# Kernel tuning notes

Measured on AMD Instinct MI355X. Metric: run time of the kernel, lower is better.

Reference implementation:

```python
import jax, jax.numpy as jnp
import numpy as np

FRACTION = 0.33  # from attn_type='query_selector_0.33'


def setup_inputs() -> dict:
    key = jax.random.key(0)
    k1, k2, k3, k4 = jax.random.split(key, 4)
    B, L, DIM_VAL, DIM_ATTN = 8, 4096, 64, 64
    scale = 1.0 / np.sqrt(DIM_VAL).astype(np.float32)
    x = jax.random.normal(k1, (B, L, DIM_VAL), dtype=jnp.float32)
    Wq = jax.random.normal(k2, (DIM_VAL, DIM_ATTN), dtype=jnp.float32) * scale
    Wk = jax.random.normal(k3, (DIM_VAL, DIM_ATTN), dtype=jnp.float32) * scale
    Wv = jax.random.normal(k4, (DIM_VAL, DIM_VAL), dtype=jnp.float32) * scale
    return {"x": x, "Wq": Wq, "Wk": Wk, "Wv": Wv}


def reference(x, Wq, Wk, Wv):
    # Projections (bias-free Linears)
    Q = jnp.einsum('bld,de->ble', x, Wq)  # [B, L, Da]
    K = jnp.einsum('bld,de->ble', x, Wk)  # [B, L, Da]
    V = jnp.einsum('bld,de->ble', x, Wv)  # [B, L, Dv]

    B, L_Q, Da = Q.shape
    l_Q = int((1.0 - FRACTION) * L_Q)  # static: shapes known at trace time

    # keys.topk(l_Q, dim=1).values -> per-channel top-l_Q along seq; mean over them
    K_top = jax.lax.top_k(jnp.swapaxes(K, 1, 2), l_Q)[0]  # [B, Da, l_Q]
    K_reduce = K_top.mean(axis=-1)                         # [B, Da]

    # score each query against the reduced key; pick top-l_Q queries
    sqk = jnp.einsum('bd,bld->bl', K_reduce, Q)            # [B, L_Q]
    indices = jax.lax.top_k(sqk, l_Q)[1]                   # [B, l_Q] int32

    # gather sampled queries
    Q_sample = jnp.take_along_axis(Q, indices[:, :, None], axis=1)  # [B, l_Q, Da]

    # dense attention for the sampled queries only
    scores = jnp.einsum('bqd,bkd->bqk', Q_sample, K) / jnp.sqrt(jnp.asarray(Da, Q.dtype))
    attn = jax.nn.softmax(scores, axis=-1)                 # [B, l_Q, L]
    out_sel = jnp.einsum('bqk,bkv->bqv', attn, V)          # [B, l_Q, Dv]

    # mean-filled result, scatter attention outputs to selected rows
    mean_values = V.mean(axis=-2)                          # [B, Dv]
    result = jnp.broadcast_to(mean_values[:, None, :], (B, L_Q, V.shape[-1]))
    result = result.at[jnp.arange(B)[:, None], indices].set(out_sel)
    return result
```

## Files before the change

kernel.cpp:

```cpp
#include <hip/hip_runtime.h>
#include <hip/hip_bf16.h>
#include <math.h>

#define BATCH 8
#define SEQ   4096
#define DIM   64
#define LQ    2744
#define QPB   128
#define NQB   22
#define QPAD  2816
#define KS    4
#define L2E   1.4426950408889634f
#define QSC   0.1803368801111204f

typedef _Float16 half8 __attribute__((ext_vector_type(8)));
typedef short    bs8   __attribute__((ext_vector_type(8)));
typedef float    fx16  __attribute__((ext_vector_type(16)));
typedef unsigned short ushort_t;

union UH { uint4 u4; half8 h; };
union UB { unsigned u[4]; uint4 u4; bs8 s; };

__device__ __forceinline__ unsigned pack_bf16(float a, float b) {
    __hip_bfloat162 h = __float22bfloat162_rn(make_float2(a, b));
    union { __hip_bfloat162 h; unsigned u; } cv; cv.h = h; return cv.u;
}

__device__ __forceinline__ unsigned f2sort(float f) {
    unsigned u = __float_as_uint(f);
    return (u & 0x80000000u) ? ~u : (u | 0x80000000u);
}
__device__ __forceinline__ float sort2f(unsigned u) {
    return __uint_as_float((u & 0x80000000u) ? (u & 0x7FFFFFFFu) : ~u);
}

__device__ void radix_select_4096(const unsigned* u, int k, unsigned* hist,
                                  unsigned* scan, unsigned* res) {
    const int t = threadIdx.x;
    if (t == 0) { res[0] = 0u; res[1] = (unsigned)k; }
    for (int pass = 3; pass >= 0; --pass) {
        const int shift = pass * 8;
        hist[t] = 0u;
        __syncthreads();
        const unsigned pref  = res[0];
        const unsigned kk    = res[1];
        const unsigned hmask = (pass == 3) ? 0u : (0xFFFFFFFFu << (shift + 8));
        for (int i = t; i < 4096; i += 256) {
            unsigned ui = u[i];
            if ((ui & hmask) == pref) atomicAdd(&hist[(ui >> shift) & 255u], 1u);
        }
        __syncthreads();
        const unsigned h = hist[t];
        unsigned s = h;
        scan[t] = s;
        __syncthreads();
#pragma unroll
        for (int ofs = 1; ofs < 256; ofs <<= 1) {
            unsigned add = (t + ofs < 256) ? scan[t + ofs] : 0u;
            __syncthreads();
            s += add;
            scan[t] = s;
            __syncthreads();
        }
        if (s >= kk && (s - h) < kk) {
            res[0] = pref | ((unsigned)t << shift);
            res[1] = kk - (s - h);
        }
        __syncthreads();
    }
}

__global__ __launch_bounds__(256) void proj_kernel(
    const float* __restrict__ x,  const float* __restrict__ Wq,
    const float* __restrict__ Wk, const float* __restrict__ Wv,
    float* __restrict__ Q, float* __restrict__ Kt,
    _Float16* __restrict__ Qh, _Float16* __restrict__ Kh,
    ushort_t* __restrict__ Vt, float* __restrict__ pmean) {
    const int rt = blockIdx.x, b = blockIdx.y, t = threadIdx.x;
    __shared__ float4 xs4[64 * 17];
    __shared__ float  red[4][64];
    {
        const float4* xg = (const float4*)(x + ((size_t)b * SEQ + rt * 64) * DIM);
        for (int i = 0; i < 4; ++i) {
            int s = t + 256 * i;
            xs4[(s >> 4) * 17 + (s & 15)] = xg[s];
        }
    }
    __syncthreads();
    const int ch = t & 63, rg = t >> 6;
    float accq[16], acck[16], accv[16];
#pragma unroll
    for (int i = 0; i < 16; ++i) { accq[i] = 0.f; acck[i] = 0.f; accv[i] = 0.f; }
    for (int dc = 0; dc < 4; ++dc) {
        float wq[16], wk[16], wv[16];
#pragma unroll
        for (int dd = 0; dd < 16; ++dd) {
            int d = dc * 16 + dd;
            wq[dd] = Wq[d * 64 + ch]; wk[dd] = Wk[d * 64 + ch]; wv[dd] = Wv[d * 64 + ch];
        }
        for (int r = 0; r < 16; ++r) {
            const int row = rg * 16 + r;
            const float4* xr = &xs4[row * 17 + dc * 4];
            float xv[16];
            float4 a0 = xr[0], a1 = xr[1], a2 = xr[2], a3 = xr[3];
            xv[0]=a0.x; xv[1]=a0.y; xv[2]=a0.z; xv[3]=a0.w;
            xv[4]=a1.x; xv[5]=a1.y; xv[6]=a1.z; xv[7]=a1.w;
            xv[8]=a2.x; xv[9]=a2.y; xv[10]=a2.z; xv[11]=a2.w;
            xv[12]=a3.x; xv[13]=a3.y; xv[14]=a3.z; xv[15]=a3.w;
#pragma unroll
            for (int dd = 0; dd < 16; ++dd) {
                accq[r] = fmaf(xv[dd], wq[dd], accq[r]);
                acck[r] = fmaf(xv[dd], wk[dd], acck[r]);
                accv[r] = fmaf(xv[dd], wv[dd], accv[r]);
            }
        }
    }
    const int rowbase = rt * 64 + rg * 16;
    float sv = 0.f;
#pragma unroll
    for (int r = 0; r < 16; ++r) {
        size_t o = ((size_t)b * SEQ + rowbase + r) * DIM + ch;
        Q[o]  = accq[r];
        Qh[o] = (_Float16)(accq[r] * QSC);
        Kh[o] = (_Float16)acck[r];
        sv += accv[r];
    }
    float4* ktp = (float4*)(Kt + ((size_t)b * 64 + ch) * SEQ + rowbase);
    ktp[0] = make_float4(acck[0], acck[1], acck[2], acck[3]);
    ktp[1] = make_float4(acck[4], acck[5], acck[6], acck[7]);
    ktp[2] = make_float4(acck[8], acck[9], acck[10], acck[11]);
    ktp[3] = make_float4(acck[12], acck[13], acck[14], acck[15]);
    {
        unsigned pk[8];
#pragma unroll
        for (int i = 0; i < 8; ++i) pk[i] = pack_bf16(accv[2*i], accv[2*i+1]);
        uint4* vp = (uint4*)(Vt + ((size_t)(b * 64 + ch)) * SEQ + rowbase);
        vp[0] = make_uint4(pk[0], pk[1], pk[4], pk[5]);
        vp[1] = make_uint4(pk[2], pk[3], pk[6], pk[7]);
    }
    red[rg][ch] = sv;
    __syncthreads();
    if (rg == 0)
        pmean[((size_t)b * 64 + ch) * 64 + rt] =
            red[0][ch] + red[1][ch] + red[2][ch] + red[3][ch];
}

__global__ __launch_bounds__(256) void kmean_kernel(const float* __restrict__ Kt,
                                                    const float* __restrict__ pmean,
                                                    float* __restrict__ Kred,
                                                    float* __restrict__ meanfin) {
    __shared__ unsigned u[4096];
    __shared__ unsigned hist[256];
    __shared__ unsigned scan[256];
    __shared__ unsigned res[2];
    __shared__ float rsum[4];
    const int bc = blockIdx.x, t = threadIdx.x;
    if (t < 64) {
        float v = pmean[(size_t)bc * 64 + t];
        for (int m = 1; m < 64; m <<= 1) v += __shfl_xor(v, m, 64);
        if (t == 0) meanfin[bc] = v * (1.0f / (float)SEQ);
    }
    const float4* c4 = (const float4*)(Kt + (size_t)bc * SEQ);
    for (int i = t; i < 1024; i += 256) {
        float4 v = c4[i];
        u[i*4+0] = f2sort(v.x); u[i*4+1] = f2sort(v.y);
        u[i*4+2] = f2sort(v.z); u[i*4+3] = f2sort(v.w);
    }
    __syncthreads();
    radix_select_4096(u, LQ, hist, scan, res);
    const unsigned Tu = res[0];
    const int krem = (int)res[1];
    float loc = 0.f;
    for (int i = t; i < 4096; i += 256)
        if (u[i] > Tu) loc += sort2f(u[i]);
    for (int msk = 1; msk < 64; msk <<= 1) loc += __shfl_xor(loc, msk, 64);
    if ((t & 63) == 0) rsum[t >> 6] = loc;
    __syncthreads();
    if (t == 0) {
        float s = rsum[0] + rsum[1] + rsum[2] + rsum[3] + (float)krem * sort2f(Tu);
        Kred[bc] = s / (float)LQ;
    }
}

__global__ __launch_bounds__(256) void sqk_kernel(const float* __restrict__ Q,
                                                  const float* __restrict__ Kred,
                                                  float* __restrict__ sqk) {
    const int b = blockIdx.y, l = blockIdx.x * 256 + threadIdx.x;
    __shared__ float kr[64];
    if (threadIdx.x < 64) kr[threadIdx.x] = Kred[b * 64 + threadIdx.x];
    __syncthreads();
    const float4* q = (const float4*)(Q + ((size_t)b * SEQ + l) * DIM);
    float s = 0.f;
#pragma unroll
    for (int i = 0; i < 16; ++i) {
        float4 v = q[i];
        s = fmaf(v.x, kr[i*4+0], s); s = fmaf(v.y, kr[i*4+1], s);
        s = fmaf(v.z, kr[i*4+2], s); s = fmaf(v.w, kr[i*4+3], s);
    }
    sqk[b * SEQ + l] = s;
}

__global__ __launch_bounds__(256) void select_kernel(const float* __restrict__ sqk,
                                                     int* __restrict__ sel,
                                                     int* __restrict__ inv) {
    __shared__ unsigned u[4096];
    __shared__ unsigned hist[256];
    __shared__ unsigned scan[256];
    __shared__ unsigned res[2];
    __shared__ int eq_idx[256];
    __shared__ int cnts[2];
    const int b = blockIdx.x, t = threadIdx.x;
    const float* col = sqk + (size_t)b * SEQ;
    int* invb = inv + (size_t)b * SEQ;
    for (int i = t; i < 4096; i += 256) {
        u[i] = f2sort(col[i]);
        invb[i] = -1;
    }
    if (t < 2) cnts[t] = 0;
    __syncthreads();
    radix_select_4096(u, LQ, hist, scan, res);
    const unsigned Tu = res[0];
    const int krem = (int)res[1];
    int* selb = sel + b * QPAD;
    for (int i = t; i < 4096; i += 256) {
        unsigned ui = u[i];
        if (ui > Tu) {
            int p = atomicAdd(&cnts[0], 1);
            selb[p] = i;
            invb[i] = p;
        } else if (ui == Tu) {
            int p = atomicAdd(&cnts[1], 1);
            if (p < 256) eq_idx[p] = i;
        }
    }
    __syncthreads();
    if (t == 0) {
        int ng = cnts[0];
        int ne = cnts[1] < 256 ? cnts[1] : 256;
        for (int i = 1; i < ne; ++i) {
            int v = eq_idx[i], j = i - 1;
            while (j >= 0 && eq_idx[j] > v) { eq_idx[j+1] = eq_idx[j]; --j; }
            eq_idx[j+1] = v;
        }
        for (int j = 0; j < krem; ++j) {
            selb[ng + j] = eq_idx[j];
            invb[eq_idx[j]] = ng + j;
        }
    }
    __syncthreads();
    if (t < QPAD - LQ) selb[LQ + t] = selb[LQ - 1];
}

__global__ __launch_bounds__(256, 3) void attn_kernel(
    const ushort_t* __restrict__ Qh, const ushort_t* __restrict__ Kh,
    const ushort_t* __restrict__ Vt, const int* __restrict__ sel,
    float* __restrict__ pl, float* __restrict__ pout) {
    const int qt = blockIdx.x, ks = blockIdx.y, b = blockIdx.z;
    const int t = threadIdx.x, w = t >> 6, lane = t & 63;
    const int col = lane & 31, h = lane >> 5;

    __shared__ ushort_t Ktile[2][32 * 64];
    __shared__ ushort_t Vtile[2][32 * 64];

    half8 qf[4];
    {
        const int q = qt * QPB + w * 32 + col;
        const int row = sel[b * QPAD + q];
        const uint4* qg = (const uint4*)(Qh + ((size_t)b * SEQ + row) * DIM);
#pragma unroll
        for (int m = 0; m < 4; ++m) { UH u; u.u4 = qg[2 * m + h]; qf[m] = u.h; }
    }

    int koff[4], voff[4];
#pragma unroll
    for (int m = 0; m < 4; ++m)
        koff[m] = col * 64 + 8 * ((2 * m + h) ^ (col & 7));
#pragma unroll
    for (int i = 0; i < 4; ++i)
        voff[i] = col * 64 + 8 * ((i * 2 + h) ^ (col & 7));

    fx16 O0, O1;
#pragma unroll
    for (int r = 0; r < 16; ++r) { O0[r] = 0.f; O1[r] = 0.f; }
    float l = 0.f;

    const int srow = t >> 3, sgr = t & 7;
    const int lg = sgr ^ (srow & 7);
    const int vD = lg >> 2, vc = (lg >> 1) & 1, vh = lg & 1;
    const size_t kgbase = ((size_t)b * SEQ + ks * 1024 + srow) * DIM + 8 * lg;
    const size_t vgbase = ((size_t)(b * DIM + srow + 32 * vD)) * SEQ
                          + ks * 1024 + vc * 16 + vh * 8;

    uint4 kreg = *(const uint4*)(Kh + kgbase);
    uint4 vreg = *(const uint4*)(Vt + vgbase);

    for (int tile = 0; tile < 32; ++tile) {
        const int buf = tile & 1;
        *(uint4*)&Ktile[buf][srow * 64 + sgr * 8] = kreg;
        *(uint4*)&Vtile[buf][srow * 64 + sgr * 8] = vreg;
        __syncthreads();
        if (tile < 31) {
            kreg = *(const uint4*)(Kh + kgbase + (size_t)(tile + 1) * 32 * DIM);
            vreg = *(const uint4*)(Vt + vgbase + (size_t)(tile + 1) * 32);
        }
        fx16 S;
#pragma unroll
        for (int r = 0; r < 16; ++r) S[r] = 0.f;
#pragma unroll
        for (int m = 0; m < 4; ++m) {
            UH kf;
            kf.u4 = *(const uint4*)&Ktile[buf][koff[m]];
            S = __builtin_amdgcn_mfma_f32_32x32x16_f16(kf.h, qf[m], S, 0, 0, 0);
        }
        float p[16];
#pragma unroll
        for (int r = 0; r < 16; ++r) p[r] = exp2f(S[r]);
#pragma unroll
        for (int r = 0; r < 16; ++r) l += p[r];
        UB A0, A1;
#pragma unroll
        for (int v = 0; v < 4; ++v) {
            A0.u[v] = pack_bf16(p[2 * v],     p[2 * v + 1]);
            A1.u[v] = pack_bf16(p[8 + 2 * v], p[8 + 2 * v + 1]);
        }
#pragma unroll
        for (int D = 0; D < 2; ++D) {
            fx16& O = D ? O1 : O0;
#pragma unroll
            for (int c = 0; c < 2; ++c) {
                UB vf;
                vf.u4 = *(const uint4*)&Vtile[buf][voff[D * 2 + c]];
                O = __builtin_amdgcn_mfma_f32_32x32x16_bf16(c ? A1.s : A0.s, vf.s, O, 0, 0, 0);
            }
        }
    }

    l += __shfl_xor(l, 32);

    const int qg0 = qt * QPB + w * 32;
    const size_t base = (size_t)b * QPAD + qg0;
#pragma unroll
    for (int D = 0; D < 2; ++D) {
        const fx16& O = D ? O1 : O0;
#pragma unroll
        for (int r = 0; r < 16; ++r) {
            const int q = (r & 3) + 8 * (r >> 2) + 4 * h;
            atomicAdd(&pout[(base + q) * DIM + D * 32 + col], O[r]);
        }
    }
    if (h == 0) atomicAdd(&pl[base + col], l);
}

__global__ __launch_bounds__(256) void comb_kernel(
    const float* __restrict__ pl, const float* __restrict__ pout,
    const int* __restrict__ inv, const float* __restrict__ meanfin,
    float* __restrict__ out) {
    const int idx = blockIdx.x * 256 + threadIdx.x;
    const int b = idx >> 16;
    const int rc = idx & 65535;
    const int row = rc >> 4, c = rc & 15;
    const int p = inv[b * SEQ + row];
    float4 o;
    if (p >= 0) {
        const size_t s0 = (size_t)b * QPAD + p;
        const float invl = 1.0f / pl[s0];
        float4 a = ((const float4*)(pout + s0 * DIM))[c];
        o = make_float4(a.x * invl, a.y * invl, a.z * invl, a.w * invl);
    } else {
        o = make_float4(meanfin[b * 64 + c * 4 + 0], meanfin[b * 64 + c * 4 + 1],
                        meanfin[b * 64 + c * 4 + 2], meanfin[b * 64 + c * 4 + 3]);
    }
    ((float4*)out)[idx] = o;
}

extern "C" void kernel_launch(void* const* d_in, const int* in_sizes, int n_in,
                              void* d_out, int out_size, void* d_ws, size_t ws_size,
                              hipStream_t stream) {
    const float* x  = (const float*)d_in[0];
    const float* Wq = (const float*)d_in[1];
    const float* Wk = (const float*)d_in[2];
    const float* Wv = (const float*)d_in[3];
    float* out = (float*)d_out;
    char* wsb  = (char*)d_ws;

    float*    Q       = (float*)(wsb);
    _Float16* Qh      = (_Float16*)(wsb + 8388608);
    _Float16* Kh      = (_Float16*)(wsb + 12582912);
    ushort_t* Vt      = (ushort_t*)(wsb + 16777216);
    float*    pmean   = (float*)(wsb + 20971520);
    float*    meanfin = (float*)(wsb + 21102592);
    float*    Kred    = (float*)(wsb + 21104640);
    float*    sqk     = (float*)(wsb + 21106688);
    int*      sel     = (int*)(wsb + 21237760);
    int*      inv     = (int*)(wsb + 21327872);
    float*    Kt      = (float*)(wsb + 21458944);
    float*    pout    = (float*)(wsb + 21458944);
    float*    pl      = (float*)(wsb + 21458944 + 5767168);

    proj_kernel  <<<dim3(64, 8),          256, 0, stream>>>(x, Wq, Wk, Wv, Q, Kt,
                                                            Qh, Kh, Vt, pmean);
    kmean_kernel <<<512,                  256, 0, stream>>>(Kt, pmean, Kred, meanfin);
    sqk_kernel   <<<dim3(16, 8),          256, 0, stream>>>(Q, Kred, sqk);
    select_kernel<<<8,                    256, 0, stream>>>(sqk, sel, inv);
    hipMemsetAsync(pout, 0, 5767168 + 90112, stream);
    attn_kernel  <<<dim3(NQB, KS, BATCH), 256, 0, stream>>>((const ushort_t*)Qh,
                                                            (const ushort_t*)Kh,
                                                            Vt, sel, pl, pout);
    comb_kernel  <<<2048,                 256, 0, stream>>>(pl, pout, inv, meanfin, out);
}
```

Baseline: 195.0 us.

## Double attention key splits, fuse query scoring into select, widen selection blocks

Raises the key-split factor from 4 to 8, so the attention grid has twice as many blocks, each covering half as many key tiles. Folds the query-scoring kernel into the selection kernel, removing one launch and the sqk buffer round trip. Runs the radix-select kernels with 1024 threads instead of 256 to speed up their histogram passes. Also swaps in a manual bf16 round-to-nearest pack and the raw exp2 builtin in the attention loop. In exchange, more atomic accumulation into the shared partial outputs, and the 8-block select kernel still has very little parallelism.

```diff
diff --git a/kernel.cpp b/kernel.cpp
--- a/kernel.cpp
+++ b/kernel.cpp
@@ -9,7 +9,7 @@
 #define QPB   128
 #define NQB   22
 #define QPAD  2816
-#define KS    4
+#define KS    8
 #define L2E   1.4426950408889634f
 #define QSC   0.1803368801111204f
 
@@ -22,8 +22,10 @@
 union UB { unsigned u[4]; uint4 u4; bs8 s; };
 
 __device__ __forceinline__ unsigned pack_bf16(float a, float b) {
-    __hip_bfloat162 h = __float22bfloat162_rn(make_float2(a, b));
-    union { __hip_bfloat162 h; unsigned u; } cv; cv.h = h; return cv.u;
+    unsigned ua = __float_as_uint(a), ub = __float_as_uint(b);
+    ua += 0x7FFFu + ((ua >> 16) & 1u);
+    ub += 0x7FFFu + ((ub >> 16) & 1u);
+    return (ua >> 16) | (ub & 0xFFFF0000u);
 }
 
 __device__ __forceinline__ unsigned f2sort(float f) {
@@ -34,35 +36,34 @@
     return __uint_as_float((u & 0x80000000u) ? (u & 0x7FFFFFFFu) : ~u);
 }
 
+template <int NT>
 __device__ void radix_select_4096(const unsigned* u, int k, unsigned* hist,
                                   unsigned* scan, unsigned* res) {
     const int t = threadIdx.x;
     if (t == 0) { res[0] = 0u; res[1] = (unsigned)k; }
     for (int pass = 3; pass >= 0; --pass) {
         const int shift = pass * 8;
-        hist[t] = 0u;
+        if (t < 256) hist[t] = 0u;
         __syncthreads();
         const unsigned pref  = res[0];
         const unsigned kk    = res[1];
         const unsigned hmask = (pass == 3) ? 0u : (0xFFFFFFFFu << (shift + 8));
-        for (int i = t; i < 4096; i += 256) {
+        for (int i = t; i < 4096; i += NT) {
             unsigned ui = u[i];
             if ((ui & hmask) == pref) atomicAdd(&hist[(ui >> shift) & 255u], 1u);
         }
         __syncthreads();
-        const unsigned h = hist[t];
-        unsigned s = h;
-        scan[t] = s;
+        unsigned h = 0u, s = 0u;
+        if (t < 256) { h = hist[t]; s = h; scan[t] = s; }
         __syncthreads();
 #pragma unroll
         for (int ofs = 1; ofs < 256; ofs <<= 1) {
-            unsigned add = (t + ofs < 256) ? scan[t + ofs] : 0u;
+            unsigned add = (t < 256 && t + ofs < 256) ? scan[t + ofs] : 0u;
             __syncthreads();
-            s += add;
-            scan[t] = s;
+            if (t < 256) { s += add; scan[t] = s; }
             __syncthreads();
         }
-        if (s >= kk && (s - h) < kk) {
+        if (t < 256 && s >= kk && (s - h) < kk) {
             res[0] = pref | ((unsigned)t << shift);
             res[1] = kk - (s - h);
         }
@@ -133,7 +134,11 @@
     {
         unsigned pk[8];
 #pragma unroll
-        for (int i = 0; i < 8; ++i) pk[i] = pack_bf16(accv[2*i], accv[2*i+1]);
+        for (int i = 0; i < 8; ++i) {
+            __hip_bfloat162 h2 = __float22bfloat162_rn(make_float2(accv[2*i], accv[2*i+1]));
+            union { __hip_bfloat162 h; unsigned u; } cv; cv.h = h2;
+            pk[i] = cv.u;
+        }
         uint4* vp = (uint4*)(Vt + ((size_t)(b * 64 + ch)) * SEQ + rowbase);
         vp[0] = make_uint4(pk[0], pk[1], pk[4], pk[5]);
         vp[1] = make_uint4(pk[2], pk[3], pk[6], pk[7]);
@@ -145,15 +150,15 @@
             red[0][ch] + red[1][ch] + red[2][ch] + red[3][ch];
 }
 
-__global__ __launch_bounds__(256) void kmean_kernel(const float* __restrict__ Kt,
-                                                    const float* __restrict__ pmean,
-                                                    float* __restrict__ Kred,
-                                                    float* __restrict__ meanfin) {
+__global__ __launch_bounds__(1024) void kmean_kernel(const float* __restrict__ Kt,
+                                                     const float* __restrict__ pmean,
+                                                     float* __restrict__ Kred,
+                                                     float* __restrict__ meanfin) {
     __shared__ unsigned u[4096];
     __shared__ unsigned hist[256];
     __shared__ unsigned scan[256];
     __shared__ unsigned res[2];
-    __shared__ float rsum[4];
+    __shared__ float rsum[16];
     const int bc = blockIdx.x, t = threadIdx.x;
     if (t < 64) {
         float v = pmean[(size_t)bc * 64 + t];
@@ -161,68 +166,62 @@
         if (t == 0) meanfin[bc] = v * (1.0f / (float)SEQ);
     }
     const float4* c4 = (const float4*)(Kt + (size_t)bc * SEQ);
-    for (int i = t; i < 1024; i += 256) {
-        float4 v = c4[i];
-        u[i*4+0] = f2sort(v.x); u[i*4+1] = f2sort(v.y);
-        u[i*4+2] = f2sort(v.z); u[i*4+3] = f2sort(v.w);
-    }
-    __syncthreads();
-    radix_select_4096(u, LQ, hist, scan, res);
+    if (t < 1024) {
+        float4 v = c4[t];
+        u[t*4+0] = f2sort(v.x); u[t*4+1] = f2sort(v.y);
+        u[t*4+2] = f2sort(v.z); u[t*4+3] = f2sort(v.w);
+    }
+    __syncthreads();
+    radix_select_4096<1024>(u, LQ, hist, scan, res);
     const unsigned Tu = res[0];
     const int krem = (int)res[1];
     float loc = 0.f;
-    for (int i = t; i < 4096; i += 256)
+    for (int i = t; i < 4096; i += 1024)
         if (u[i] > Tu) loc += sort2f(u[i]);
     for (int msk = 1; msk < 64; msk <<= 1) loc += __shfl_xor(loc, msk, 64);
     if ((t & 63) == 0) rsum[t >> 6] = loc;
     __syncthreads();
     if (t == 0) {
-        float s = rsum[0] + rsum[1] + rsum[2] + rsum[3] + (float)krem * sort2f(Tu);
+        float s = (float)krem * sort2f(Tu);
+        for (int i = 0; i < 16; ++i) s += rsum[i];
         Kred[bc] = s / (float)LQ;
     }
 }
 
-__global__ __launch_bounds__(256) void sqk_kernel(const float* __restrict__ Q,
-                                                  const float* __restrict__ Kred,
-                                                  float* __restrict__ sqk) {
-    const int b = blockIdx.y, l = blockIdx.x * 256 + threadIdx.x;
-    __shared__ float kr[64];
-    if (threadIdx.x < 64) kr[threadIdx.x] = Kred[b * 64 + threadIdx.x];
-    __syncthreads();
-    const float4* q = (const float4*)(Q + ((size_t)b * SEQ + l) * DIM);
-    float s = 0.f;
-#pragma unroll
-    for (int i = 0; i < 16; ++i) {
-        float4 v = q[i];
-        s = fmaf(v.x, kr[i*4+0], s); s = fmaf(v.y, kr[i*4+1], s);
-        s = fmaf(v.z, kr[i*4+2], s); s = fmaf(v.w, kr[i*4+3], s);
-    }
-    sqk[b * SEQ + l] = s;
-}
-
-__global__ __launch_bounds__(256) void select_kernel(const float* __restrict__ sqk,
-                                                     int* __restrict__ sel,
-                                                     int* __restrict__ inv) {
+__global__ __launch_bounds__(1024) void select_kernel(const float* __restrict__ Q,
+                                                      const float* __restrict__ Kred,
+                                                      int* __restrict__ sel,
+                                                      int* __restrict__ inv) {
     __shared__ unsigned u[4096];
     __shared__ unsigned hist[256];
     __shared__ unsigned scan[256];
     __shared__ unsigned res[2];
+    __shared__ float kr[64];
     __shared__ int eq_idx[256];
     __shared__ int cnts[2];
     const int b = blockIdx.x, t = threadIdx.x;
-    const float* col = sqk + (size_t)b * SEQ;
+    if (t < 64) kr[t] = Kred[b * 64 + t];
+    if (t < 2) cnts[t] = 0;
     int* invb = inv + (size_t)b * SEQ;
-    for (int i = t; i < 4096; i += 256) {
-        u[i] = f2sort(col[i]);
-        invb[i] = -1;
-    }
-    if (t < 2) cnts[t] = 0;
-    __syncthreads();
-    radix_select_4096(u, LQ, hist, scan, res);
+    __syncthreads();
+    for (int row = t; row < 4096; row += 1024) {
+        const float4* q = (const float4*)(Q + ((size_t)b * SEQ + row) * DIM);
+        float s = 0.f;
+#pragma unroll
+        for (int i = 0; i < 16; ++i) {
+            float4 v = q[i];
+            s = fmaf(v.x, kr[i*4+0], s); s = fmaf(v.y, kr[i*4+1], s);
+            s = fmaf(v.z, kr[i*4+2], s); s = fmaf(v.w, kr[i*4+3], s);
+        }
+        u[row] = f2sort(s);
+        invb[row] = -1;
+    }
+    __syncthreads();
+    radix_select_4096<1024>(u, LQ, hist, scan, res);
     const unsigned Tu = res[0];
     const int krem = (int)res[1];
     int* selb = sel + b * QPAD;
-    for (int i = t; i < 4096; i += 256) {
+    for (int i = t; i < 4096; i += 1024) {
         unsigned ui = u[i];
         if (ui > Tu) {
             int p = atomicAdd(&cnts[0], 1);
@@ -287,19 +286,19 @@
     const int srow = t >> 3, sgr = t & 7;
     const int lg = sgr ^ (srow & 7);
     const int vD = lg >> 2, vc = (lg >> 1) & 1, vh = lg & 1;
-    const size_t kgbase = ((size_t)b * SEQ + ks * 1024 + srow) * DIM + 8 * lg;
+    const size_t kgbase = ((size_t)b * SEQ + ks * 512 + srow) * DIM + 8 * lg;
     const size_t vgbase = ((size_t)(b * DIM + srow + 32 * vD)) * SEQ
-                          + ks * 1024 + vc * 16 + vh * 8;
+                          + ks * 512 + vc * 16 + vh * 8;
 
     uint4 kreg = *(const uint4*)(Kh + kgbase);
     uint4 vreg = *(const uint4*)(Vt + vgbase);
 
-    for (int tile = 0; tile < 32; ++tile) {
+    for (int tile = 0; tile < 16; ++tile) {
         const int buf = tile & 1;
         *(uint4*)&Ktile[buf][srow * 64 + sgr * 8] = kreg;
         *(uint4*)&Vtile[buf][srow * 64 + sgr * 8] = vreg;
         __syncthreads();
-        if (tile < 31) {
+        if (tile < 15) {
             kreg = *(const uint4*)(Kh + kgbase + (size_t)(tile + 1) * 32 * DIM);
             vreg = *(const uint4*)(Vt + vgbase + (size_t)(tile + 1) * 32);
         }
@@ -314,7 +313,7 @@
         }
         float p[16];
 #pragma unroll
-        for (int r = 0; r < 16; ++r) p[r] = exp2f(S[r]);
+        for (int r = 0; r < 16; ++r) p[r] = __builtin_amdgcn_exp2f(S[r]);
 #pragma unroll
         for (int r = 0; r < 16; ++r) l += p[r];
         UB A0, A1;
@@ -390,21 +389,19 @@
     float*    pmean   = (float*)(wsb + 20971520);
     float*    meanfin = (float*)(wsb + 21102592);
     float*    Kred    = (float*)(wsb + 21104640);
-    float*    sqk     = (float*)(wsb + 21106688);
-    int*      sel     = (int*)(wsb + 21237760);
-    int*      inv     = (int*)(wsb + 21327872);
-    float*    Kt      = (float*)(wsb + 21458944);
-    float*    pout    = (float*)(wsb + 21458944);
-    float*    pl      = (float*)(wsb + 21458944 + 5767168);
-
-    proj_kernel  <<<dim3(64, 8),          256, 0, stream>>>(x, Wq, Wk, Wv, Q, Kt,
-                                                            Qh, Kh, Vt, pmean);
-    kmean_kernel <<<512,                  256, 0, stream>>>(Kt, pmean, Kred, meanfin);
-    sqk_kernel   <<<dim3(16, 8),          256, 0, stream>>>(Q, Kred, sqk);
-    select_kernel<<<8,                    256, 0, stream>>>(sqk, sel, inv);
+    int*      sel     = (int*)(wsb + 21106688);
+    int*      inv     = (int*)(wsb + 21196800);
+    float*    Kt      = (float*)(wsb + 21327872);
+    float*    pout    = (float*)(wsb + 21327872);
+    float*    pl      = (float*)(wsb + 21327872 + 5767168);
+
+    proj_kernel  <<<dim3(64, 8),          256,  0, stream>>>(x, Wq, Wk, Wv, Q, Kt,
+                                                             Qh, Kh, Vt, pmean);
+    kmean_kernel <<<512,                  1024, 0, stream>>>(Kt, pmean, Kred, meanfin);
+    select_kernel<<<8,                    1024, 0, stream>>>(Q, Kred, sel, inv);
     hipMemsetAsync(pout, 0, 5767168 + 90112, stream);
-    attn_kernel  <<<dim3(NQB, KS, BATCH), 256, 0, stream>>>((const ushort_t*)Qh,
-                                                            (const ushort_t*)Kh,
-                                                            Vt, sel, pl, pout);
-    comb_kernel  <<<2048,                 256, 0, stream>>>(pl, pout, inv, meanfin, out);
-}
+    attn_kernel  <<<dim3(NQB, KS, BATCH), 256,  0, stream>>>((const ushort_t*)Qh,
+                                                             (const ushort_t*)Kh,
+                                                             Vt, sel, pl, pout);
+    comb_kernel  <<<2048,                 256,  0, stream>>>(pl, pout, inv, meanfin, out);
+}
```

Measured after the change: 220.6 us. 1.13x slower.
